# Optimization experiments

Measured on AMD Instinct MI355X. Metric: run time of the kernel, lower is better.

Reference implementation:

```python
import jax, jax.numpy as jnp
import numpy as np

N_EMB = 384
BLOCK_SIZE = 256


def setup_inputs() -> dict:
    key = jax.random.key(0)
    ks = jax.random.split(key, 6)
    B, T, H, D = 256, 256, 6, 64
    x = jax.random.normal(ks[0], (B, T, N_EMB), dtype=jnp.float32)
    wk = jax.random.normal(ks[1], (H, N_EMB, D), dtype=jnp.float32) * (N_EMB ** -0.5)
    wq = jax.random.normal(ks[2], (H, N_EMB, D), dtype=jnp.float32) * (N_EMB ** -0.5)
    wv = jax.random.normal(ks[3], (H, N_EMB, D), dtype=jnp.float32) * (N_EMB ** -0.5)
    wproj = jax.random.normal(ks[4], (N_EMB, N_EMB), dtype=jnp.float32) * (N_EMB ** -0.5)
    bproj = jnp.zeros((N_EMB,), dtype=jnp.float32)
    return {"x": x, "wk": wk, "wq": wq, "wv": wv, "wproj": wproj, "bproj": bproj}


def reference(x, wk, wq, wv, wproj, bproj):
    B, T, C = x.shape  # C == N_EMB
    # per-head projections (no bias), heads stacked on leading axis
    k = jnp.einsum('btc,hcd->bhtd', x, wk)
    q = jnp.einsum('btc,hcd->bhtd', x, wq)
    v = jnp.einsum('btc,hcd->bhtd', x, wv)
    # faithful to source: wei = k @ q^T scaled by sqrt(C) (embed dim, not head dim)
    wei = jnp.einsum('bhtd,bhsd->bhts', k, q) / (C ** 0.5)
    causal = jnp.tril(jnp.ones((T, T), dtype=bool))
    wei = jnp.where(causal, wei, -jnp.inf)
    wei = jax.nn.softmax(wei, axis=-1)
    # dropout is identity in eval mode
    out = jnp.einsum('bhts,bhsd->bhtd', wei, v)  # [B,H,T,D]
    out = out.transpose(0, 2, 1, 3).reshape(B, T, C)  # concat heads
    out = out @ wproj + bproj
    return out
```

## Files before the change

### kernel.cpp

```cpp
#include <hip/hip_runtime.h>

typedef unsigned short u16;
typedef __bf16 bf16x8 __attribute__((ext_vector_type(8)));
typedef float f32x4 __attribute__((ext_vector_type(4)));

#define B_SZ 256
#define T_SZ 256
#define C_EMB 384
#define NHEAD 6
#define DHEAD 64
#define N3 1152
#define BHTD 25165824
#define SCALE 0.05103103630798287f

__device__ __forceinline__ u16 f2bf(float f) {
  unsigned u = __float_as_uint(f);
  u += 0x7FFFu + ((u >> 16) & 1u);
  return (u16)(u >> 16);
}

__device__ __forceinline__ void gload_lds16(const void* g, void* l) {
  __builtin_amdgcn_global_load_lds((const __attribute__((address_space(1))) void*)g,
                                   (__attribute__((address_space(3))) void*)l, 16, 0, 0);
}

__global__ __launch_bounds__(256) void prep_weights(
    const float* __restrict__ wk, const float* __restrict__ wq,
    const float* __restrict__ wv, const float* __restrict__ wproj,
    u16* __restrict__ wqkvt, u16* __restrict__ wprojt) {
  int i = blockIdx.x * 256 + threadIdx.x;
  if (i < N3 * C_EMB) {
    int n = i / C_EMB, c = i - n * C_EMB;
    int tensor = n >= 768 ? 2 : (n >= 384 ? 1 : 0);
    int r = n - tensor * 384;
    int h = r >> 6, d = r & 63;
    const float* w = tensor == 0 ? wk : (tensor == 1 ? wq : wv);
    float val = w[(h * C_EMB + c) * DHEAD + d];
    if (tensor == 0) val *= SCALE;
    wqkvt[i] = f2bf(val);
  } else {
    int ii = i - N3 * C_EMB;
    if (ii < C_EMB * C_EMB) {
      int n = ii / C_EMB, c = ii - n * C_EMB;
      wprojt[ii] = f2bf(wproj[c * C_EMB + n]);
    }
  }
}

__global__ __launch_bounds__(256) void prep_x(const float* __restrict__ x,
                                              u16* __restrict__ xb) {
  int i = blockIdx.x * 256 + threadIdx.x;
  float4 f0 = ((const float4*)x)[i * 2];
  float4 f1 = ((const float4*)x)[i * 2 + 1];
  uint4 p;
  p.x = (unsigned)f2bf(f0.x) | ((unsigned)f2bf(f0.y) << 16);
  p.y = (unsigned)f2bf(f0.z) | ((unsigned)f2bf(f0.w) << 16);
  p.z = (unsigned)f2bf(f1.x) | ((unsigned)f2bf(f1.y) << 16);
  p.w = (unsigned)f2bf(f1.z) | ((unsigned)f2bf(f1.w) << 16);
  ((uint4*)xb)[i] = p;
}

__global__ __launch_bounds__(256) void qkv_gemm(const u16* __restrict__ xb,
                                                const u16* __restrict__ wt,
                                                u16* __restrict__ kqv) {
  __shared__ __align__(16) u16 lA[2][128 * 64];
  __shared__ __align__(16) u16 lB[2][128 * 64];
  const int tid = threadIdx.x;
  const int lane = tid & 63, w = tid >> 6;
  int bid = blockIdx.x;
  int nb = (bid & 7) * 576 + (bid >> 3);
  int mt = nb / 9, nt = nb - mt * 9;
  const int n0 = nt * 128, m0 = mt * 128;
  const int wr = w >> 1, wc = w & 1;
  f32x4 acc[4][4] = {};

#define QSTAGE(buf, kt_) { \
    int k0_ = (kt_) * 64; \
    _Pragma("unroll") for (int it = 0; it < 4; ++it) { \
      int ub = it * 256 + w * 64; int u = ub + lane; \
      int row = u >> 3, cu = u & 7; \
      int koff = k0_ + ((cu ^ (row & 7)) << 3); \
      gload_lds16(xb + (size_t)(m0 + row) * C_EMB + koff, lA[buf] + ub * 8); \
      gload_lds16(wt + (size_t)(n0 + row) * C_EMB + koff, lB[buf] + ub * 8); \
    } }

  QSTAGE(0, 0);
  int cur = 0;
  for (int kt = 0; kt < 6; ++kt) {
    if (kt < 5) {
      QSTAGE(cur ^ 1, kt + 1);
      asm volatile("s_waitcnt vmcnt(8)" ::: "memory");
    } else {
      asm volatile("s_waitcnt vmcnt(0)" ::: "memory");
    }
    asm volatile("s_barrier" ::: "memory");
    bf16x8 af[4][2], bfr[4][2];
#pragma unroll
    for (int mi = 0; mi < 4; ++mi) {
      int row = wr * 64 + mi * 16 + (lane & 15);
#pragma unroll
      for (int kk = 0; kk < 2; ++kk) {
        int cu = kk * 4 + (lane >> 4);
        af[mi][kk] = *(const bf16x8*)((const char*)lA[cur] + row * 128 + ((cu ^ (row & 7)) << 4));
      }
    }
#pragma unroll
    for (int ni = 0; ni < 4; ++ni) {
      int row = wc * 64 + ni * 16 + (lane & 15);
#pragma unroll
      for (int kk = 0; kk < 2; ++kk) {
        int cu = kk * 4 + (lane >> 4);
        bfr[ni][kk] = *(const bf16x8*)((const char*)lB[cur] + row * 128 + ((cu ^ (row & 7)) << 4));
      }
    }
#pragma unroll
    for (int kk = 0; kk < 2; ++kk)
#pragma unroll
      for (int mi = 0; mi < 4; ++mi)
#pragma unroll
        for (int ni = 0; ni < 4; ++ni)
          acc[mi][ni] = __builtin_amdgcn_mfma_f32_16x16x32_bf16(
              af[mi][kk], bfr[ni][kk], acc[mi][ni], 0, 0, 0);
    asm volatile("s_barrier" ::: "memory");
    cur ^= 1;
  }
#undef QSTAGE

  const int tensor = nt / 3;
  if (tensor == 2) {
    u16* vt = kqv + 2 * (size_t)BHTD;
#pragma unroll
    for (int ni = 0; ni < 4; ++ni) {
      int r2 = n0 + wc * 64 + ni * 16 + (lane & 15) - 768;
      int h = r2 >> 6, d = r2 & 63;
#pragma unroll
      for (int mi = 0; mi < 4; ++mi) {
        int gm0 = m0 + wr * 64 + mi * 16 + ((lane >> 4) << 2);
        int b = gm0 >> 8, tt = gm0 & 255;
        ushort4 pk;
        pk.x = f2bf(acc[mi][ni][0]);
        pk.y = f2bf(acc[mi][ni][1]);
        pk.z = f2bf(acc[mi][ni][2]);
        pk.w = f2bf(acc[mi][ni][3]);
        *(ushort4*)(vt + ((size_t)(b * NHEAD + h) * 64 + d) * 256 + tt) = pk;
      }
    }
  } else {
#pragma unroll
    for (int ni = 0; ni < 4; ++ni) {
      int gn = n0 + wc * 64 + ni * 16 + (lane & 15);
      int r2 = gn - tensor * 384;
      int h = r2 >> 6, d = r2 & 63;
#pragma unroll
      for (int mi = 0; mi < 4; ++mi) {
        int gm0 = m0 + wr * 64 + mi * 16 + ((lane >> 4) << 2);
#pragma unroll
        for (int r = 0; r < 4; ++r) {
          int m = gm0 + r;
          int b = m >> 8, t = m & 255;
          kqv[(size_t)tensor * BHTD + ((((b * NHEAD + h) << 8) + t) << 6) + d] =
              f2bf(acc[mi][ni][r]);
        }
      }
    }
  }
}

__global__ __launch_bounds__(512, 4) void attn_kernel(const u16* __restrict__ kqv,
                                                      u16* __restrict__ attnb) {
  __shared__ __align__(16) u16 lK[128 * 64];
  __shared__ __align__(16) u16 lQ[2][64 * 64];
  __shared__ __align__(16) u16 lVt[2][64 * 64];
  __shared__ __align__(16) char lP[8 * 16 * 144];
  const int tid = threadIdx.x;
  const int lane = tid & 63, w = tid >> 6;
  int bid = blockIdx.x;
  int id = (bid & 7) * 384 + (bid >> 3);
  const int bh = id >> 1, tt = id & 1;
  const int t0 = tt * 128;
  const u16* Kb = kqv + (size_t)bh * (T_SZ * DHEAD);
  const u16* Qb = kqv + (size_t)BHTD + (size_t)bh * (T_SZ * DHEAD);
  const u16* Vb = kqv + 2 * (size_t)BHTD + (size_t)bh * (DHEAD * T_SZ);

#define STAGE_Q(buf, ss) { int ub = w * 64; int u = ub + lane; \
    int row = u >> 3, cu = u & 7; \
    gload_lds16(Qb + (size_t)((ss) + row) * DHEAD + ((cu ^ (row & 7)) << 3), lQ[buf] + ub * 8); }
#define STAGE_V(buf, ss) { int ub = w * 64; int u = ub + lane; \
    int row = u >> 3, cu = u & 7; \
    gload_lds16(Vb + (size_t)row * T_SZ + (ss) + ((cu ^ (row & 7)) << 3), lVt[buf] + ub * 8); }

#pragma unroll
  for (int it = 0; it < 2; ++it) {
    int ub = it * 512 + w * 64;
    int u = ub + lane;
    int row = u >> 3, cu = u & 7;
    gload_lds16(Kb + (size_t)(t0 + row) * DHEAD + ((cu ^ (row & 7)) << 3), lK + ub * 8);
  }
  STAGE_Q(0, 0);
  STAGE_V(0, 0);
  asm volatile("s_waitcnt vmcnt(2)" ::: "memory");
  asm volatile("s_barrier" ::: "memory");

  const int t0w = t0 + w * 16;
  const int tg0 = t0w + ((lane >> 4) << 2);
  bf16x8 af[2];
  {
    int arow = w * 16 + (lane & 15);
#pragma unroll
    for (int kk = 0; kk < 2; ++kk) {
      int cu = kk * 4 + (lane >> 4);
      af[kk] = *(const bf16x8*)((const char*)lK + arow * 128 + ((cu ^ (arow & 7)) << 4));
    }
  }
  char* lPw = lP + w * (16 * 144);
  f32x4 oacc[4] = {};
  float mrow[4] = {-1e30f, -1e30f, -1e30f, -1e30f};
  float lrowp[4] = {0.f, 0.f, 0.f, 0.f};
  const int nst = 2 * tt + 2;
  int cur = 0;
  for (int si = 0; si < nst; ++si) {
    const int s0 = si << 6;
    if (si + 1 < nst) {
      STAGE_Q(cur ^ 1, s0 + 64);
      STAGE_V(cur ^ 1, s0 + 64);
      asm volatile("s_waitcnt vmcnt(2)" ::: "memory");
    } else {
      asm volatile("s_waitcnt vmcnt(0)" ::: "memory");
    }
    asm volatile("s_barrier" ::: "memory");
    if (s0 <= t0w + 15) {
      f32x4 sacc[4] = {};
#pragma unroll
      for (int ni = 0; ni < 4; ++ni) {
        int row = ni * 16 + (lane & 15);
#pragma unroll
        for (int kk = 0; kk < 2; ++kk) {
          int cu = kk * 4 + (lane >> 4);
          bf16x8 bq = *(const bf16x8*)((const char*)lQ[cur] + row * 128 + ((cu ^ (row & 7)) << 4));
          sacc[ni] = __builtin_amdgcn_mfma_f32_16x16x32_bf16(af[kk], bq, sacc[ni], 0, 0, 0);
        }
      }
      float pm[4][4];
      float rmax[4] = {-1e30f, -1e30f, -1e30f, -1e30f};
      if (s0 + 63 > t0w) {
#pragma unroll
        for (int ni = 0; ni < 4; ++ni) {
          int sg = s0 + ni * 16 + (lane & 15);
#pragma unroll
          for (int r = 0; r < 4; ++r) {
            float vv = sacc[ni][r];
            if (sg > tg0 + r) vv = -1e30f;
            pm[ni][r] = vv;
            rmax[r] = fmaxf(rmax[r], vv);
          }
        }
      } else {
#pragma unroll
        for (int ni = 0; ni < 4; ++ni)
#pragma unroll
          for (int r = 0; r < 4; ++r) {
            float vv = sacc[ni][r];
            pm[ni][r] = vv;
            rmax[r] = fmaxf(rmax[r], vv);
          }
      }
#pragma unroll
      for (int r = 0; r < 4; ++r) {
#pragma unroll
        for (int off = 1; off < 16; off <<= 1)
          rmax[r] = fmaxf(rmax[r], __shfl_xor(rmax[r], off));
      }
      bool small = (rmax[0] - mrow[0] <= 8.f) && (rmax[1] - mrow[1] <= 8.f) &&
                   (rmax[2] - mrow[2] <= 8.f) && (rmax[3] - mrow[3] <= 8.f);
      if (!__all(small)) {
#pragma unroll
        for (int r = 0; r < 4; ++r) {
          float mnew = fmaxf(mrow[r], rmax[r]);
          float alpha = __expf(mrow[r] - mnew);
          mrow[r] = mnew;
          lrowp[r] *= alpha;
#pragma unroll
          for (int nd = 0; nd < 4; ++nd) oacc[nd][r] *= alpha;
        }
      }
#pragma unroll
      for (int ni = 0; ni < 4; ++ni)
#pragma unroll
        for (int r = 0; r < 4; ++r) {
          float p = __expf(pm[ni][r] - mrow[r]);
          pm[ni][r] = p;
          lrowp[r] += p;
        }
#pragma unroll
      for (int ni = 0; ni < 4; ++ni) {
        int scol = ni * 16 + (lane & 15);
#pragma unroll
        for (int r = 0; r < 4; ++r) {
          int trow = ((lane >> 4) << 2) + r;
          *(u16*)(lPw + trow * 144 + scol * 2) = f2bf(pm[ni][r]);
        }
      }
      bf16x8 pa[2];
      {
        int trow = lane & 15;
#pragma unroll
        for (int kk = 0; kk < 2; ++kk) {
          int cu = kk * 4 + (lane >> 4);
          pa[kk] = *(const bf16x8*)(lPw + trow * 144 + cu * 16);
        }
      }
#pragma unroll
      for (int nd = 0; nd < 4; ++nd) {
        int drow = nd * 16 + (lane & 15);
#pragma unroll
        for (int kk = 0; kk < 2; ++kk) {
          int cu = kk * 4 + (lane >> 4);
          bf16x8 vb = *(const bf16x8*)((const char*)lVt[cur] + drow * 128 + ((cu ^ (drow & 7)) << 4));
          oacc[nd] = __builtin_amdgcn_mfma_f32_16x16x32_bf16(pa[kk], vb, oacc[nd], 0, 0, 0);
        }
      }
    }
    asm volatile("s_barrier" ::: "memory");
    cur ^= 1;
  }
#undef STAGE_Q
#undef STAGE_V
#pragma unroll
  for (int r = 0; r < 4; ++r) {
#pragma unroll
    for (int off = 1; off < 16; off <<= 1)
      lrowp[r] += __shfl_xor(lrowp[r], off);
  }
  const int b = bh / NHEAD, h = bh - (bh / NHEAD) * NHEAD;
#pragma unroll
  for (int r = 0; r < 4; ++r) {
    int t = tg0 + r;
    float inv = 1.0f / lrowp[r];
#pragma unroll
    for (int nd = 0; nd < 4; ++nd) {
      int col = h * 64 + nd * 16 + (lane & 15);
      attnb[((size_t)(b * T_SZ + t)) * C_EMB + col] = f2bf(oacc[nd][r] * inv);
    }
  }
}

__global__ __launch_bounds__(256) void out_gemm(const u16* __restrict__ a,
                                                const u16* __restrict__ wt,
                                                const float* __restrict__ bias,
                                                float* __restrict__ out) {
  __shared__ __align__(16) u16 lA[2][128 * 64];
  __shared__ __align__(16) u16 lB[2][128 * 64];
  const int tid = threadIdx.x;
  const int lane = tid & 63, w = tid >> 6;
  int bid = blockIdx.x;
  int nb = (bid & 7) * 192 + (bid >> 3);
  int mt = nb / 3, nt = nb - mt * 3;
  const int n0 = nt * 128, m0 = mt * 128;
  const int wr = w >> 1, wc = w & 1;
  f32x4 acc[4][4] = {};

#define OSTAGE(buf, kt_) { \
    int k0_ = (kt_) * 64; \
    _Pragma("unroll") for (int it = 0; it < 4; ++it) { \
      int ub = it * 256 + w * 64; int u = ub + lane; \
      int row = u >> 3, cu = u & 7; \
      int koff = k0_ + ((cu ^ (row & 7)) << 3); \
      gload_lds16(a + (size_t)(m0 + row) * C_EMB + koff, lA[buf] + ub * 8); \
      gload_lds16(wt + (size_t)(n0 + row) * C_EMB + koff, lB[buf] + ub * 8); \
    } }

  OSTAGE(0, 0);
  int cur = 0;
  for (int kt = 0; kt < 6; ++kt) {
    if (kt < 5) {
      OSTAGE(cur ^ 1, kt + 1);
      asm volatile("s_waitcnt vmcnt(8)" ::: "memory");
    } else {
      asm volatile("s_waitcnt vmcnt(0)" ::: "memory");
    }
    asm volatile("s_barrier" ::: "memory");
    bf16x8 af[4][2], bfr[4][2];
#pragma unroll
    for (int mi = 0; mi < 4; ++mi) {
      int row = wr * 64 + mi * 16 + (lane & 15);
#pragma unroll
      for (int kk = 0; kk < 2; ++kk) {
        int cu = kk * 4 + (lane >> 4);
        af[mi][kk] = *(const bf16x8*)((const char*)lA[cur] + row * 128 + ((cu ^ (row & 7)) << 4));
      }
    }
#pragma unroll
    for (int ni = 0; ni < 4; ++ni) {
      int row = wc * 64 + ni * 16 + (lane & 15);
#pragma unroll
      for (int kk = 0; kk < 2; ++kk) {
        int cu = kk * 4 + (lane >> 4);
        bfr[ni][kk] = *(const bf16x8*)((const char*)lB[cur] + row * 128 + ((cu ^ (row & 7)) << 4));
      }
    }
#pragma unroll
    for (int kk = 0; kk < 2; ++kk)
#pragma unroll
      for (int mi = 0; mi < 4; ++mi)
#pragma unroll
        for (int ni = 0; ni < 4; ++ni)
          acc[mi][ni] = __builtin_amdgcn_mfma_f32_16x16x32_bf16(
              af[mi][kk], bfr[ni][kk], acc[mi][ni], 0, 0, 0);
    asm volatile("s_barrier" ::: "memory");
    cur ^= 1;
  }
#undef OSTAGE
#pragma unroll
  for (int ni = 0; ni < 4; ++ni) {
    int gn = n0 + wc * 64 + ni * 16 + (lane & 15);
    float bv = bias[gn];
#pragma unroll
    for (int mi = 0; mi < 4; ++mi) {
      int gm0 = m0 + wr * 64 + mi * 16 + ((lane >> 4) << 2);
#pragma unroll
      for (int r = 0; r < 4; ++r)
        out[(size_t)(gm0 + r) * C_EMB + gn] = acc[mi][ni][r] + bv;
    }
  }
}

extern "C" void kernel_launch(void* const* d_in, const int* in_sizes, int n_in,
                              void* d_out, int out_size, void* d_ws, size_t ws_size,
                              hipStream_t stream) {
  const float* x = (const float*)d_in[0];
  const float* wk = (const float*)d_in[1];
  const float* wq = (const float*)d_in[2];
  const float* wv = (const float*)d_in[3];
  const float* wproj = (const float*)d_in[4];
  const float* bproj = (const float*)d_in[5];
  float* out = (float*)d_out;
  u16* ws = (u16*)d_ws;
  u16* kqv = ws;
  u16* attnb = ws + 3 * (size_t)BHTD;
  u16* xb = attnb;
  u16* wqkvt = attnb + (size_t)BHTD;
  u16* wprojt = wqkvt + (size_t)N3 * C_EMB;
  prep_weights<<<2304, 256, 0, stream>>>(wk, wq, wv, wproj, wqkvt, wprojt);
  prep_x<<<12288, 256, 0, stream>>>(x, xb);
  qkv_gemm<<<4608, 256, 0, stream>>>(xb, wqkvt, kqv);
  attn_kernel<<<3072, 512, 0, stream>>>(kqv, attnb);
  out_gemm<<<1536, 256, 0, stream>>>(attnb, wprojt, bproj, out);
}
```

Measured before the change: 206.8 us.

## Retile QKV and output GEMMs to 512x128 tiles with 8 waves and BK=32

Both bf16 GEMMs now use 512-thread blocks computing 512x128 output tiles with a K-step of 32 instead of 128x128 tiles with K-step 64. Each wave holds an 8x4 MFMA accumulator grid, and the LDS swizzle becomes a 4-chunk XOR pattern. Reusing each B tile across four times as many rows cuts global and L2 traffic per output element. In exchange there are twice as many K iterations and barriers, higher register pressure, and far fewer blocks (1152 and 384), which may underfill the GPU for the output GEMM.

```diff
diff --git a/kernel.cpp b/kernel.cpp
--- a/kernel.cpp
+++ b/kernel.cpp
@@ -12,6 +12,8 @@
 #define N3 1152
 #define BHTD 25165824
 #define SCALE 0.05103103630798287f
+
+#define SW4(r) ((((r) >> 2) ^ (r)) & 3)
 
 __device__ __forceinline__ u16 f2bf(float f) {
   unsigned u = __float_as_uint(f);
@@ -60,100 +62,92 @@
   ((uint4*)xb)[i] = p;
 }
 
-__global__ __launch_bounds__(256) void qkv_gemm(const u16* __restrict__ xb,
+__global__ __launch_bounds__(512) void qkv_gemm(const u16* __restrict__ xb,
                                                 const u16* __restrict__ wt,
                                                 u16* __restrict__ kqv) {
-  __shared__ __align__(16) u16 lA[2][128 * 64];
-  __shared__ __align__(16) u16 lB[2][128 * 64];
+  __shared__ __align__(16) u16 lA[2][512 * 32];
+  __shared__ __align__(16) u16 lB[2][128 * 32];
   const int tid = threadIdx.x;
   const int lane = tid & 63, w = tid >> 6;
   int bid = blockIdx.x;
-  int nb = (bid & 7) * 576 + (bid >> 3);
-  int mt = nb / 9, nt = nb - mt * 9;
-  const int n0 = nt * 128, m0 = mt * 128;
+  int id = (bid & 7) * 144 + (bid >> 3);
+  int mt = id / 9, nt = id - mt * 9;
+  const int m0 = mt * 512, n0 = nt * 128;
   const int wr = w >> 1, wc = w & 1;
-  f32x4 acc[4][4] = {};
+  f32x4 acc[8][4] = {};
 
 #define QSTAGE(buf, kt_) { \
-    int k0_ = (kt_) * 64; \
+    int k0_ = (kt_) * 32; \
     _Pragma("unroll") for (int it = 0; it < 4; ++it) { \
-      int ub = it * 256 + w * 64; int u = ub + lane; \
-      int row = u >> 3, cu = u & 7; \
-      int koff = k0_ + ((cu ^ (row & 7)) << 3); \
-      gload_lds16(xb + (size_t)(m0 + row) * C_EMB + koff, lA[buf] + ub * 8); \
-      gload_lds16(wt + (size_t)(n0 + row) * C_EMB + koff, lB[buf] + ub * 8); \
-    } }
+      int u = it * 512 + tid; int row = u >> 2, cu = u & 3; \
+      gload_lds16(xb + (size_t)(m0 + row) * C_EMB + k0_ + ((cu ^ SW4(row)) << 3), \
+                  lA[buf] + u * 8); \
+    } \
+    { int u = tid; int row = u >> 2, cu = u & 3; \
+      gload_lds16(wt + (size_t)(n0 + row) * C_EMB + k0_ + ((cu ^ SW4(row)) << 3), \
+                  lB[buf] + u * 8); } }
 
   QSTAGE(0, 0);
   int cur = 0;
-  for (int kt = 0; kt < 6; ++kt) {
-    if (kt < 5) {
+  for (int kt = 0; kt < 12; ++kt) {
+    if (kt < 11) {
       QSTAGE(cur ^ 1, kt + 1);
-      asm volatile("s_waitcnt vmcnt(8)" ::: "memory");
+      asm volatile("s_waitcnt vmcnt(5)" ::: "memory");
     } else {
       asm volatile("s_waitcnt vmcnt(0)" ::: "memory");
     }
     asm volatile("s_barrier" ::: "memory");
-    bf16x8 af[4][2], bfr[4][2];
-#pragma unroll
-    for (int mi = 0; mi < 4; ++mi) {
-      int row = wr * 64 + mi * 16 + (lane & 15);
-#pragma unroll
-      for (int kk = 0; kk < 2; ++kk) {
-        int cu = kk * 4 + (lane >> 4);
-        af[mi][kk] = *(const bf16x8*)((const char*)lA[cur] + row * 128 + ((cu ^ (row & 7)) << 4));
-      }
+    bf16x8 af[8], bfr[4];
+#pragma unroll
+    for (int mi = 0; mi < 8; ++mi) {
+      int row = wr * 128 + mi * 16 + (lane & 15);
+      int cu = (lane >> 4) ^ SW4(row);
+      af[mi] = *(const bf16x8*)((const char*)lA[cur] + row * 64 + cu * 16);
     }
 #pragma unroll
     for (int ni = 0; ni < 4; ++ni) {
       int row = wc * 64 + ni * 16 + (lane & 15);
-#pragma unroll
-      for (int kk = 0; kk < 2; ++kk) {
-        int cu = kk * 4 + (lane >> 4);
-        bfr[ni][kk] = *(const bf16x8*)((const char*)lB[cur] + row * 128 + ((cu ^ (row & 7)) << 4));
-      }
-    }
-#pragma unroll
-    for (int kk = 0; kk < 2; ++kk)
-#pragma unroll
-      for (int mi = 0; mi < 4; ++mi)
-#pragma unroll
-        for (int ni = 0; ni < 4; ++ni)
-          acc[mi][ni] = __builtin_amdgcn_mfma_f32_16x16x32_bf16(
-              af[mi][kk], bfr[ni][kk], acc[mi][ni], 0, 0, 0);
+      int cu = (lane >> 4) ^ SW4(row);
+      bfr[ni] = *(const bf16x8*)((const char*)lB[cur] + row * 64 + cu * 16);
+    }
+#pragma unroll
+    for (int mi = 0; mi < 8; ++mi)
+#pragma unroll
+      for (int ni = 0; ni < 4; ++ni)
+        acc[mi][ni] = __builtin_amdgcn_mfma_f32_16x16x32_bf16(
+            af[mi], bfr[ni], acc[mi][ni], 0, 0, 0);
     asm volatile("s_barrier" ::: "memory");
     cur ^= 1;
   }
 #undef QSTAGE
 
-  const int tensor = nt / 3;
+  const int tensor = nt / 3, ntt = nt - tensor * 3;
   if (tensor == 2) {
     u16* vt = kqv + 2 * (size_t)BHTD;
 #pragma unroll
     for (int ni = 0; ni < 4; ++ni) {
-      int r2 = n0 + wc * 64 + ni * 16 + (lane & 15) - 768;
+      int r2 = ntt * 128 + wc * 64 + ni * 16 + (lane & 15);
       int h = r2 >> 6, d = r2 & 63;
 #pragma unroll
-      for (int mi = 0; mi < 4; ++mi) {
-        int gm0 = m0 + wr * 64 + mi * 16 + ((lane >> 4) << 2);
-        int b = gm0 >> 8, tt = gm0 & 255;
+      for (int mi = 0; mi < 8; ++mi) {
+        int gm0 = m0 + wr * 128 + mi * 16 + ((lane >> 4) << 2);
+        int b = gm0 >> 8, tt2 = gm0 & 255;
         ushort4 pk;
         pk.x = f2bf(acc[mi][ni][0]);
         pk.y = f2bf(acc[mi][ni][1]);
         pk.z = f2bf(acc[mi][ni][2]);
         pk.w = f2bf(acc[mi][ni][3]);
-        *(ushort4*)(vt + ((size_t)(b * NHEAD + h) * 64 + d) * 256 + tt) = pk;
+        *(ushort4*)(vt + ((size_t)(b * NHEAD + h) * 64 + d) * 256 + tt2) = pk;
       }
     }
   } else {
 #pragma unroll
     for (int ni = 0; ni < 4; ++ni) {
-      int gn = n0 + wc * 64 + ni * 16 + (lane & 15);
-      int r2 = gn - tensor * 384;
+      int r2 = ntt * 128 + wc * 64 + ni * 16 + (lane & 15);
       int h = r2 >> 6, d = r2 & 63;
 #pragma unroll
-      for (int mi = 0; mi < 4; ++mi) {
-        int gm0 = m0 + wr * 64 + mi * 16 + ((lane >> 4) << 2);
+      for (int mi = 0; mi < 8; ++mi) {
+        int gm0 = m0 + wr * 128 + mi * 16 + ((lane >> 4) << 2);
 #pragma unroll
         for (int r = 0; r < 4; ++r) {
           int m = gm0 + r;
@@ -344,68 +338,61 @@
   }
 }
 
-__global__ __launch_bounds__(256) void out_gemm(const u16* __restrict__ a,
+__global__ __launch_bounds__(512) void out_gemm(const u16* __restrict__ a,
                                                 const u16* __restrict__ wt,
                                                 const float* __restrict__ bias,
                                                 float* __restrict__ out) {
-  __shared__ __align__(16) u16 lA[2][128 * 64];
-  __shared__ __align__(16) u16 lB[2][128 * 64];
+  __shared__ __align__(16) u16 lA[2][512 * 32];
+  __shared__ __align__(16) u16 lB[2][128 * 32];
   const int tid = threadIdx.x;
   const int lane = tid & 63, w = tid >> 6;
   int bid = blockIdx.x;
-  int nb = (bid & 7) * 192 + (bid >> 3);
-  int mt = nb / 3, nt = nb - mt * 3;
-  const int n0 = nt * 128, m0 = mt * 128;
+  int id = (bid & 7) * 48 + (bid >> 3);
+  int mt = id / 3, nt = id - mt * 3;
+  const int m0 = mt * 512, n0 = nt * 128;
   const int wr = w >> 1, wc = w & 1;
-  f32x4 acc[4][4] = {};
+  f32x4 acc[8][4] = {};
 
 #define OSTAGE(buf, kt_) { \
-    int k0_ = (kt_) * 64; \
+    int k0_ = (kt_) * 32; \
     _Pragma("unroll") for (int it = 0; it < 4; ++it) { \
-      int ub = it * 256 + w * 64; int u = ub + lane; \
-      int row = u >> 3, cu = u & 7; \
-      int koff = k0_ + ((cu ^ (row & 7)) << 3); \
-      gload_lds16(a + (size_t)(m0 + row) * C_EMB + koff, lA[buf] + ub * 8); \
-      gload_lds16(wt + (size_t)(n0 + row) * C_EMB + koff, lB[buf] + ub * 8); \
-    } }
+      int u = it * 512 + tid; int row = u >> 2, cu = u & 3; \
+      gload_lds16(a + (size_t)(m0 + row) * C_EMB + k0_ + ((cu ^ SW4(row)) << 3), \
+                  lA[buf] + u * 8); \
+    } \
+    { int u = tid; int row = u >> 2, cu = u & 3; \
+      gload_lds16(wt + (size_t)(n0 + row) * C_EMB + k0_ + ((cu ^ SW4(row)) << 3), \
+                  lB[buf] + u * 8); } }
 
   OSTAGE(0, 0);
   int cur = 0;
-  for (int kt = 0; kt < 6; ++kt) {
-    if (kt < 5) {
+  for (int kt = 0; kt < 12; ++kt) {
+    if (kt < 11) {
       OSTAGE(cur ^ 1, kt + 1);
-      asm volatile("s_waitcnt vmcnt(8)" ::: "memory");
+      asm volatile("s_waitcnt vmcnt(5)" ::: "memory");
     } else {
       asm volatile("s_waitcnt vmcnt(0)" ::: "memory");
     }
     asm volatile("s_barrier" ::: "memory");
-    bf16x8 af[4][2], bfr[4][2];
-#pragma unroll
-    for (int mi = 0; mi < 4; ++mi) {
-      int row = wr * 64 + mi * 16 + (lane & 15);
-#pragma unroll
-      for (int kk = 0; kk < 2; ++kk) {
-        int cu = kk * 4 + (lane >> 4);
-        af[mi][kk] = *(const bf16x8*)((const char*)lA[cur] + row * 128 + ((cu ^ (row & 7)) << 4));
-      }
+    bf16x8 af[8], bfr[4];
+#pragma unroll
+    for (int mi = 0; mi < 8; ++mi) {
+      int row = wr * 128 + mi * 16 + (lane & 15);
+      int cu = (lane >> 4) ^ SW4(row);
+      af[mi] = *(const bf16x8*)((const char*)lA[cur] + row * 64 + cu * 16);
     }
 #pragma unroll
     for (int ni = 0; ni < 4; ++ni) {
       int row = wc * 64 + ni * 16 + (lane & 15);
-#pragma unroll
-      for (int kk = 0; kk < 2; ++kk) {
-        int cu = kk * 4 + (lane >> 4);
-        bfr[ni][kk] = *(const bf16x8*)((const char*)lB[cur] + row * 128 + ((cu ^ (row & 7)) << 4));
-      }
-    }
-#pragma unroll
-    for (int kk = 0; kk < 2; ++kk)
-#pragma unroll
-      for (int mi = 0; mi < 4; ++mi)
-#pragma unroll
-        for (int ni = 0; ni < 4; ++ni)
-          acc[mi][ni] = __builtin_amdgcn_mfma_f32_16x16x32_bf16(
-              af[mi][kk], bfr[ni][kk], acc[mi][ni], 0, 0, 0);
+      int cu = (lane >> 4) ^ SW4(row);
+      bfr[ni] = *(const bf16x8*)((const char*)lB[cur] + row * 64 + cu * 16);
+    }
+#pragma unroll
+    for (int mi = 0; mi < 8; ++mi)
+#pragma unroll
+      for (int ni = 0; ni < 4; ++ni)
+        acc[mi][ni] = __builtin_amdgcn_mfma_f32_16x16x32_bf16(
+            af[mi], bfr[ni], acc[mi][ni], 0, 0, 0);
     asm volatile("s_barrier" ::: "memory");
     cur ^= 1;
   }
@@ -415,8 +402,8 @@
     int gn = n0 + wc * 64 + ni * 16 + (lane & 15);
     float bv = bias[gn];
 #pragma unroll
-    for (int mi = 0; mi < 4; ++mi) {
-      int gm0 = m0 + wr * 64 + mi * 16 + ((lane >> 4) << 2);
+    for (int mi = 0; mi < 8; ++mi) {
+      int gm0 = m0 + wr * 128 + mi * 16 + ((lane >> 4) << 2);
 #pragma unroll
       for (int r = 0; r < 4; ++r)
         out[(size_t)(gm0 + r) * C_EMB + gn] = acc[mi][ni][r] + bv;
@@ -442,7 +429,7 @@
   u16* wprojt = wqkvt + (size_t)N3 * C_EMB;
   prep_weights<<<2304, 256, 0, stream>>>(wk, wq, wv, wproj, wqkvt, wprojt);
   prep_x<<<12288, 256, 0, stream>>>(x, xb);
-  qkv_gemm<<<4608, 256, 0, stream>>>(xb, wqkvt, kqv);
+  qkv_gemm<<<1152, 512, 0, stream>>>(xb, wqkvt, kqv);
   attn_kernel<<<3072, 512, 0, stream>>>(kqv, attnb);
-  out_gemm<<<1536, 256, 0, stream>>>(attnb, wprojt, bproj, out);
-}
+  out_gemm<<<384, 512, 0, stream>>>(attnb, wprojt, bproj, out);
+}
```

Result: slower. 243.0 us (+17.5%).
